# Optimization experiments

Hardware: AMD Instinct MI355X
Metric: run time of the kernel (lower is better)

## Reference

```python
import jax, jax.numpy as jnp
import numpy as np

B, I, J, DIN, DOUT = 256, 1152, 10, 8, 16
ROUTING_ITERS = 3


def squash(v):
    # v: [..., D]; squash(v) = (|v|^2 / (1+|v|^2)) * v/|v| = v * |v| / (1+|v|^2)
    l2 = jnp.linalg.norm(v, axis=-1, keepdims=True)
    return v * (l2 / (1.0 + l2 * l2))


def setup_inputs() -> dict:
    key = jax.random.key(0)
    k1, k2 = jax.random.split(key)
    x = jax.random.normal(k1, (B, I, DIN), dtype=jnp.float32)
    # per-(i,j) Linear(DIN -> DOUT, bias=False) weights, stacked: [I, J, DOUT, DIN]
    W = jax.random.normal(k2, (I, J, DOUT, DIN), dtype=jnp.float32) * 0.1
    return {"x": x, "W": W}


def reference(x, W):
    # prediction vectors u[b,i,j,:] = W[i,j] @ x[b,i,:]  -> [B, I, J, DOUT]
    u = jnp.einsum('bid,ijod->bijo', x, W)
    b = jnp.zeros((I, J), dtype=u.dtype)  # routing logits (shared across batch)
    s = None
    for _ in range(ROUTING_ITERS):
        c = jax.nn.softmax(b, axis=-1)              # [I, J]
        s = jnp.einsum('ij,bijd->bjd', c, u)        # coupling-weighted sum over in-caps
        s = squash(s)                               # [B, J, DOUT]
        # agreement: b[i,j] += sum_b <u[b,i,j], s[b,j]>
        b = b + jnp.einsum('bijd,bjd->ij', u, s)
    return s
```

## Files before the change

### kernel.cpp

```cpp
#include <hip/hip_runtime.h>
#include <math.h>

typedef unsigned short ushort_t;
typedef __attribute__((ext_vector_type(8))) __bf16 bf16x8;
typedef __attribute__((ext_vector_type(4))) float floatx4;

#define B_    256
#define I_    1152
#define J_    10
#define DIN_  8
#define DOUT_ 16
#define K_    (I_*DIN_)
#define N_    (J_*DOUT_)
#define WPS   16
#define KCHUNK (K_/WPS)
#define KSTEPS (KCHUNK/32)

static __device__ __forceinline__ ushort_t f2bf(float f) {
    unsigned int u = __float_as_uint(f);
    u += 0x7fffu + ((u >> 16) & 1u);
    return (ushort_t)(u >> 16);
}
static __device__ __forceinline__ float bf2f(ushort_t h) {
    return __uint_as_float(((unsigned int)h) << 16);
}

__global__ __launch_bounds__(1024)
void gemm_s_fused_kernel(const float* __restrict__ x, const float* __restrict__ W,
                         const float* __restrict__ blog, float* __restrict__ s_out,
                         ushort_t* __restrict__ Sbt_hi, ushort_t* __restrict__ Sbt_lo,
                         const int iter)
{
    const int tid  = threadIdx.x;
    const int tile = blockIdx.x;
    const int lane = tid & 63;
    const int w    = tid >> 6;
    const int mb   = tile / J_;
    const int nt   = tile - mb * J_;

    __shared__ float  c_lds[I_];
    __shared__ floatx4 part[WPS * 64];

    if (iter > 0) {
        for (int r2 = tid; r2 < I_; r2 += 1024) {
            const float* br = blog + (size_t)r2 * J_;
            float bv[J_];
            float mx = -1e30f;
            #pragma unroll
            for (int j = 0; j < J_; ++j) { bv[j] = br[j]; mx = fmaxf(mx, bv[j]); }
            float sum = 0.f;
            #pragma unroll
            for (int j = 0; j < J_; ++j) { bv[j] = __expf(bv[j] - mx); sum += bv[j]; }
            c_lds[r2] = bv[nt] / sum;
        }
        __syncthreads();
    }

    {
        const int r = lane & 15, q = lane >> 4;
        const float* ap = x + (size_t)(mb * 16 + r) * K_ + w * KCHUNK + 8 * q;
        const float* wp = W + (((size_t)(w * 72 + q) * J_ + nt) * DOUT_ + r) * DIN_;
        floatx4 acc = {0.f, 0.f, 0.f, 0.f};
        #pragma unroll
        for (int s = 0; s < KSTEPS; ++s) {
            float4 xa0 = *(const float4*)(ap + s * 32);
            float4 xa1 = *(const float4*)(ap + s * 32 + 4);
            float4 w0  = *(const float4*)(wp + (size_t)s * 4 * J_ * DOUT_ * DIN_);
            float4 w1  = *(const float4*)(wp + (size_t)s * 4 * J_ * DOUT_ * DIN_ + 4);
            float cs   = (iter == 0) ? 0.1f : c_lds[w * 72 + 4 * s + q];
            float xv[8]  = {xa0.x, xa0.y, xa0.z, xa0.w, xa1.x, xa1.y, xa1.z, xa1.w};
            float wvv[8] = {w0.x, w0.y, w0.z, w0.w, w1.x, w1.y, w1.z, w1.w};
            bf16x8 ah, al, bh, bl;
            #pragma unroll
            for (int e = 0; e < 8; ++e) {
                float xe = xv[e];
                __bf16 h = (__bf16)xe;
                ah[e] = h;
                al[e] = (__bf16)(xe - (float)h);
                float pe = wvv[e] * cs;
                __bf16 g = (__bf16)pe;
                bh[e] = g;
                bl[e] = (__bf16)(pe - (float)g);
            }
            acc = __builtin_amdgcn_mfma_f32_16x16x32_bf16(ah, bh, acc, 0, 0, 0);
            acc = __builtin_amdgcn_mfma_f32_16x16x32_bf16(al, bh, acc, 0, 0, 0);
            acc = __builtin_amdgcn_mfma_f32_16x16x32_bf16(ah, bl, acc, 0, 0, 0);
        }
        part[w * 64 + lane] = acc;
    }
    __syncthreads();

    if (tid < 256) {
        const int b_local = tid >> 4;
        const int o       = tid & 15;
        const int lane_c  = ((b_local >> 2) << 4) | o;
        const int reg     = b_local & 3;
        float v = 0.f;
        #pragma unroll
        for (int u = 0; u < WPS; ++u)
            v += part[u * 64 + lane_c][reg];
        float sq = v * v;
        #pragma unroll
        for (int off = 1; off < 16; off <<= 1)
            sq += __shfl_xor(sq, off, 16);
        float l2 = sqrtf(sq);
        float val = v * (l2 / (1.f + sq));
        const int b  = mb * 16 + b_local;
        const int jo = nt * 16 + o;
        if (iter == 2) {
            s_out[(size_t)b * N_ + jo] = val;
        } else {
            ushort_t hi = f2bf(val);
            Sbt_hi[(size_t)jo * B_ + b] = hi;
            Sbt_lo[(size_t)jo * B_ + b] = f2bf(val - bf2f(hi));
        }
    }
}

__global__ __launch_bounds__(256)
void gemm_bupd_kernel(const float* __restrict__ x,
                      const ushort_t* __restrict__ Sbt_hi, const ushort_t* __restrict__ Sbt_lo,
                      const float* __restrict__ W, float* __restrict__ blog,
                      const int first)
{
    int wv   = blockIdx.x * 4 + (threadIdx.x >> 6);
    int lane = threadIdx.x & 63;
    int mt = wv / J_;
    int j  = wv - mt * J_;
    int r = lane & 15, q = lane >> 4;
    const float* xp = x + (size_t)(8 * q) * K_ + (mt * 16 + r);
    size_t boff = (size_t)(j * 16 + r) * B_ + 8 * q;
    floatx4 acc = {0.f, 0.f, 0.f, 0.f};
    #pragma unroll
    for (int s = 0; s < B_ / 32; ++s) {
        bf16x8 ah, al;
        #pragma unroll
        for (int e = 0; e < 8; ++e) {
            float v = xp[(size_t)(s * 32 + e) * K_];
            __bf16 h = (__bf16)v;
            ah[e] = h;
            al[e] = (__bf16)(v - (float)h);
        }
        bf16x8 bh = *(const bf16x8*)(Sbt_hi + boff + s * 32);
        bf16x8 bl = *(const bf16x8*)(Sbt_lo + boff + s * 32);
        acc = __builtin_amdgcn_mfma_f32_16x16x32_bf16(ah, bh, acc, 0, 0, 0);
        acc = __builtin_amdgcn_mfma_f32_16x16x32_bf16(al, bh, acc, 0, 0, 0);
        acc = __builtin_amdgcn_mfma_f32_16x16x32_bf16(ah, bl, acc, 0, 0, 0);
    }
    int i  = mt * 2 + (q >> 1);
    int d0 = (q & 1) * 4;
    int o  = lane & 15;
    const float4 w4 = *(const float4*)(W + ((((size_t)i * J_ + j) * DOUT_ + o) * DIN_ + d0));
    float val = acc[0] * w4.x + acc[1] * w4.y + acc[2] * w4.z + acc[3] * w4.w;
    #pragma unroll
    for (int off = 1; off < 32; off <<= 1)
        val += __shfl_xor(val, off, 32);
    if ((lane & 31) == 0) {
        float* dst = blog + (size_t)(mt * 2 + (lane >> 5)) * J_ + j;
        if (first) *dst = val; else *dst += val;
    }
}

extern "C" void kernel_launch(void* const* d_in, const int* in_sizes, int n_in,
                              void* d_out, int out_size, void* d_ws, size_t ws_size,
                              hipStream_t stream)
{
    const float* x = (const float*)d_in[0];
    const float* W = (const float*)d_in[1];
    float* s_out = (float*)d_out;

    char* ws = (char*)d_ws;
    ushort_t* Sbt_hi = (ushort_t*)(ws);
    ushort_t* Sbt_lo = (ushort_t*)(ws + 81920);
    float*    blog   = (float*)   (ws + 163840);

    for (int it = 0; it < 3; ++it) {
        gemm_s_fused_kernel<<<160, 1024, 0, stream>>>(x, W, blog, s_out,
                                                      Sbt_hi, Sbt_lo, it);
        if (it < 2)
            gemm_bupd_kernel<<<1440, 256, 0, stream>>>(x, Sbt_hi, Sbt_lo,
                                                       W, blog, it == 0 ? 1 : 0);
    }
}
```

Before: 163.3 us.

## Cache bf16-split W across routing iterations and pair j outputs in bupd

```diff
diff --git a/kernel.cpp b/kernel.cpp
--- a/kernel.cpp
+++ b/kernel.cpp
@@ -29,6 +29,7 @@
 void gemm_s_fused_kernel(const float* __restrict__ x, const float* __restrict__ W,
                          const float* __restrict__ blog, float* __restrict__ s_out,
                          ushort_t* __restrict__ Sbt_hi, ushort_t* __restrict__ Sbt_lo,
+                         ushort_t* __restrict__ Wt_hi, ushort_t* __restrict__ Wt_lo,
                          const int iter)
 {
     const int tid  = threadIdx.x;
@@ -60,31 +61,57 @@
         const int r = lane & 15, q = lane >> 4;
         const float* ap = x + (size_t)(mb * 16 + r) * K_ + w * KCHUNK + 8 * q;
         const float* wp = W + (((size_t)(w * 72 + q) * J_ + nt) * DOUT_ + r) * DIN_;
+        const size_t wtoff = (size_t)(nt * 16 + r) * K_ + w * KCHUNK + 8 * q;
         floatx4 acc = {0.f, 0.f, 0.f, 0.f};
-        #pragma unroll
-        for (int s = 0; s < KSTEPS; ++s) {
-            float4 xa0 = *(const float4*)(ap + s * 32);
-            float4 xa1 = *(const float4*)(ap + s * 32 + 4);
-            float4 w0  = *(const float4*)(wp + (size_t)s * 4 * J_ * DOUT_ * DIN_);
-            float4 w1  = *(const float4*)(wp + (size_t)s * 4 * J_ * DOUT_ * DIN_ + 4);
-            float cs   = (iter == 0) ? 0.1f : c_lds[w * 72 + 4 * s + q];
-            float xv[8]  = {xa0.x, xa0.y, xa0.z, xa0.w, xa1.x, xa1.y, xa1.z, xa1.w};
-            float wvv[8] = {w0.x, w0.y, w0.z, w0.w, w1.x, w1.y, w1.z, w1.w};
-            bf16x8 ah, al, bh, bl;
-            #pragma unroll
-            for (int e = 0; e < 8; ++e) {
-                float xe = xv[e];
-                __bf16 h = (__bf16)xe;
-                ah[e] = h;
-                al[e] = (__bf16)(xe - (float)h);
-                float pe = wvv[e] * cs;
-                __bf16 g = (__bf16)pe;
-                bh[e] = g;
-                bl[e] = (__bf16)(pe - (float)g);
+
+        if (iter == 0) {
+            #pragma unroll
+            for (int s = 0; s < KSTEPS; ++s) {
+                float4 xa0 = *(const float4*)(ap + s * 32);
+                float4 xa1 = *(const float4*)(ap + s * 32 + 4);
+                float4 w0  = *(const float4*)(wp + (size_t)s * 4 * J_ * DOUT_ * DIN_);
+                float4 w1  = *(const float4*)(wp + (size_t)s * 4 * J_ * DOUT_ * DIN_ + 4);
+                float xv[8]  = {xa0.x, xa0.y, xa0.z, xa0.w, xa1.x, xa1.y, xa1.z, xa1.w};
+                float wvv[8] = {w0.x, w0.y, w0.z, w0.w, w1.x, w1.y, w1.z, w1.w};
+                bf16x8 ah, al, bh, bl;
+                #pragma unroll
+                for (int e = 0; e < 8; ++e) {
+                    float xe = xv[e] * 0.1f;
+                    __bf16 h = (__bf16)xe;
+                    ah[e] = h;
+                    al[e] = (__bf16)(xe - (float)h);
+                    float pe = wvv[e];
+                    __bf16 g = (__bf16)pe;
+                    bh[e] = g;
+                    bl[e] = (__bf16)(pe - (float)g);
+                }
+                *(bf16x8*)(Wt_hi + wtoff + s * 32) = bh;
+                *(bf16x8*)(Wt_lo + wtoff + s * 32) = bl;
+                acc = __builtin_amdgcn_mfma_f32_16x16x32_bf16(ah, bh, acc, 0, 0, 0);
+                acc = __builtin_amdgcn_mfma_f32_16x16x32_bf16(al, bh, acc, 0, 0, 0);
+                acc = __builtin_amdgcn_mfma_f32_16x16x32_bf16(ah, bl, acc, 0, 0, 0);
             }
-            acc = __builtin_amdgcn_mfma_f32_16x16x32_bf16(ah, bh, acc, 0, 0, 0);
-            acc = __builtin_amdgcn_mfma_f32_16x16x32_bf16(al, bh, acc, 0, 0, 0);
-            acc = __builtin_amdgcn_mfma_f32_16x16x32_bf16(ah, bl, acc, 0, 0, 0);
+        } else {
+            #pragma unroll
+            for (int s = 0; s < KSTEPS; ++s) {
+                float4 xa0 = *(const float4*)(ap + s * 32);
+                float4 xa1 = *(const float4*)(ap + s * 32 + 4);
+                bf16x8 bh = *(const bf16x8*)(Wt_hi + wtoff + s * 32);
+                bf16x8 bl = *(const bf16x8*)(Wt_lo + wtoff + s * 32);
+                float cs  = c_lds[w * 72 + 4 * s + q];
+                float xv[8] = {xa0.x, xa0.y, xa0.z, xa0.w, xa1.x, xa1.y, xa1.z, xa1.w};
+                bf16x8 ah, al;
+                #pragma unroll
+                for (int e = 0; e < 8; ++e) {
+                    float xe = xv[e] * cs;
+                    __bf16 h = (__bf16)xe;
+                    ah[e] = h;
+                    al[e] = (__bf16)(xe - (float)h);
+                }
+                acc = __builtin_amdgcn_mfma_f32_16x16x32_bf16(ah, bh, acc, 0, 0, 0);
+                acc = __builtin_amdgcn_mfma_f32_16x16x32_bf16(al, bh, acc, 0, 0, 0);
+                acc = __builtin_amdgcn_mfma_f32_16x16x32_bf16(ah, bl, acc, 0, 0, 0);
+            }
         }
         part[w * 64 + lane] = acc;
     }
@@ -125,12 +152,15 @@
 {
     int wv   = blockIdx.x * 4 + (threadIdx.x >> 6);
     int lane = threadIdx.x & 63;
-    int mt = wv / J_;
-    int j  = wv - mt * J_;
+    int mt = wv / 5;
+    int jp = wv - mt * 5;
+    int j0 = jp * 2, j1 = jp * 2 + 1;
     int r = lane & 15, q = lane >> 4;
     const float* xp = x + (size_t)(8 * q) * K_ + (mt * 16 + r);
-    size_t boff = (size_t)(j * 16 + r) * B_ + 8 * q;
-    floatx4 acc = {0.f, 0.f, 0.f, 0.f};
+    size_t b0off = (size_t)(j0 * 16 + r) * B_ + 8 * q;
+    size_t b1off = (size_t)(j1 * 16 + r) * B_ + 8 * q;
+    floatx4 acc0 = {0.f, 0.f, 0.f, 0.f};
+    floatx4 acc1 = {0.f, 0.f, 0.f, 0.f};
     #pragma unroll
     for (int s = 0; s < B_ / 32; ++s) {
         bf16x8 ah, al;
@@ -141,23 +171,42 @@
             ah[e] = h;
             al[e] = (__bf16)(v - (float)h);
         }
-        bf16x8 bh = *(const bf16x8*)(Sbt_hi + boff + s * 32);
-        bf16x8 bl = *(const bf16x8*)(Sbt_lo + boff + s * 32);
-        acc = __builtin_amdgcn_mfma_f32_16x16x32_bf16(ah, bh, acc, 0, 0, 0);
-        acc = __builtin_amdgcn_mfma_f32_16x16x32_bf16(al, bh, acc, 0, 0, 0);
-        acc = __builtin_amdgcn_mfma_f32_16x16x32_bf16(ah, bl, acc, 0, 0, 0);
+        bf16x8 bh0 = *(const bf16x8*)(Sbt_hi + b0off + s * 32);
+        bf16x8 bl0 = *(const bf16x8*)(Sbt_lo + b0off + s * 32);
+        bf16x8 bh1 = *(const bf16x8*)(Sbt_hi + b1off + s * 32);
+        bf16x8 bl1 = *(const bf16x8*)(Sbt_lo + b1off + s * 32);
+        acc0 = __builtin_amdgcn_mfma_f32_16x16x32_bf16(ah, bh0, acc0, 0, 0, 0);
+        acc0 = __builtin_amdgcn_mfma_f32_16x16x32_bf16(al, bh0, acc0, 0, 0, 0);
+        acc0 = __builtin_amdgcn_mfma_f32_16x16x32_bf16(ah, bl0, acc0, 0, 0, 0);
+        acc1 = __builtin_amdgcn_mfma_f32_16x16x32_bf16(ah, bh1, acc1, 0, 0, 0);
+        acc1 = __builtin_amdgcn_mfma_f32_16x16x32_bf16(al, bh1, acc1, 0, 0, 0);
+        acc1 = __builtin_amdgcn_mfma_f32_16x16x32_bf16(ah, bl1, acc1, 0, 0, 0);
     }
     int i  = mt * 2 + (q >> 1);
     int d0 = (q & 1) * 4;
     int o  = lane & 15;
-    const float4 w4 = *(const float4*)(W + ((((size_t)i * J_ + j) * DOUT_ + o) * DIN_ + d0));
-    float val = acc[0] * w4.x + acc[1] * w4.y + acc[2] * w4.z + acc[3] * w4.w;
-    #pragma unroll
-    for (int off = 1; off < 32; off <<= 1)
-        val += __shfl_xor(val, off, 32);
-    if ((lane & 31) == 0) {
-        float* dst = blog + (size_t)(mt * 2 + (lane >> 5)) * J_ + j;
-        if (first) *dst = val; else *dst += val;
+    int iw = mt * 2 + (lane >> 5);
+    {
+        const float4 w4 = *(const float4*)(W + ((((size_t)i * J_ + j0) * DOUT_ + o) * DIN_ + d0));
+        float val = acc0[0] * w4.x + acc0[1] * w4.y + acc0[2] * w4.z + acc0[3] * w4.w;
+        #pragma unroll
+        for (int off = 1; off < 32; off <<= 1)
+            val += __shfl_xor(val, off, 32);
+        if ((lane & 31) == 0) {
+            float* dst = blog + (size_t)iw * J_ + j0;
+            if (first) *dst = val; else *dst += val;
+        }
+    }
+    {
+        const float4 w4 = *(const float4*)(W + ((((size_t)i * J_ + j1) * DOUT_ + o) * DIN_ + d0));
+        float val = acc1[0] * w4.x + acc1[1] * w4.y + acc1[2] * w4.z + acc1[3] * w4.w;
+        #pragma unroll
+        for (int off = 1; off < 32; off <<= 1)
+            val += __shfl_xor(val, off, 32);
+        if ((lane & 31) == 0) {
+            float* dst = blog + (size_t)iw * J_ + j1;
+            if (first) *dst = val; else *dst += val;
+        }
     }
 }
 
@@ -173,12 +222,15 @@
     ushort_t* Sbt_hi = (ushort_t*)(ws);
     ushort_t* Sbt_lo = (ushort_t*)(ws + 81920);
     float*    blog   = (float*)   (ws + 163840);
+    ushort_t* Wt_hi  = (ushort_t*)(ws + 209920);
+    ushort_t* Wt_lo  = (ushort_t*)(ws + 3159040);
 
     for (int it = 0; it < 3; ++it) {
         gemm_s_fused_kernel<<<160, 1024, 0, stream>>>(x, W, blog, s_out,
-                                                      Sbt_hi, Sbt_lo, it);
+                                                      Sbt_hi, Sbt_lo,
+                                                      Wt_hi, Wt_lo, it);
         if (it < 2)
-            gemm_bupd_kernel<<<1440, 256, 0, stream>>>(x, Sbt_hi, Sbt_lo,
-                                                       W, blog, it == 0 ? 1 : 0);
-    }
-}
+            gemm_bupd_kernel<<<720, 256, 0, stream>>>(x, Sbt_hi, Sbt_lo,
+                                                      W, blog, it == 0 ? 1 : 0);
+    }
+}
```

Result: slower. 199.6 us (+22.2%).

## Fuse routing-logit update into s-computation kernel with atomic accumulation

Applied to the files above, without the earlier changes.

```diff
diff --git a/kernel.cpp b/kernel.cpp
--- a/kernel.cpp
+++ b/kernel.cpp
@@ -26,9 +26,8 @@
 }
 
 __global__ __launch_bounds__(1024)
-void gemm_s_fused_kernel(const float* __restrict__ x, const float* __restrict__ W,
-                         const float* __restrict__ blog, float* __restrict__ s_out,
-                         ushort_t* __restrict__ Sbt_hi, ushort_t* __restrict__ Sbt_lo,
+void capsule_iter_kernel(const float* __restrict__ x, const float* __restrict__ W,
+                         float* __restrict__ blog, float* __restrict__ s_out,
                          const int iter)
 {
     const int tid  = threadIdx.x;
@@ -37,9 +36,12 @@
     const int w    = tid >> 6;
     const int mb   = tile / J_;
     const int nt   = tile - mb * J_;
+    const int b0   = mb * 16;
+    const int r    = lane & 15, q = lane >> 4;
 
-    __shared__ float  c_lds[I_];
+    __shared__ float   c_lds[I_];
     __shared__ floatx4 part[WPS * 64];
+    __shared__ float   s_lds[16 * 16];
 
     if (iter > 0) {
         for (int r2 = tid; r2 < I_; r2 += 1024) {
@@ -57,7 +59,6 @@
     }
 
     {
-        const int r = lane & 15, q = lane >> 4;
         const float* ap = x + (size_t)(mb * 16 + r) * K_ + w * KCHUNK + 8 * q;
         const float* wp = W + (((size_t)(w * 72 + q) * J_ + nt) * DOUT_ + r) * DIN_;
         floatx4 acc = {0.f, 0.f, 0.f, 0.f};
@@ -105,59 +106,60 @@
             sq += __shfl_xor(sq, off, 16);
         float l2 = sqrtf(sq);
         float val = v * (l2 / (1.f + sq));
-        const int b  = mb * 16 + b_local;
-        const int jo = nt * 16 + o;
-        if (iter == 2) {
-            s_out[(size_t)b * N_ + jo] = val;
-        } else {
-            ushort_t hi = f2bf(val);
-            Sbt_hi[(size_t)jo * B_ + b] = hi;
-            Sbt_lo[(size_t)jo * B_ + b] = f2bf(val - bf2f(hi));
+        if (iter == 2)
+            s_out[(size_t)(b0 + b_local) * N_ + nt * 16 + o] = val;
+        else
+            s_lds[b_local * 16 + o] = val;
+    }
+
+    if (iter == 2) return;
+    __syncthreads();
+
+    {
+        bf16x8 bh, bl;
+        #pragma unroll
+        for (int e = 0; e < 8; ++e) { bh[e] = (__bf16)0.f; bl[e] = (__bf16)0.f; }
+        if (q < 2) {
+            #pragma unroll
+            for (int e = 0; e < 8; ++e) {
+                float sv = s_lds[(8 * q + e) * 16 + r];
+                __bf16 h = (__bf16)sv;
+                bh[e] = h;
+                bl[e] = (__bf16)(sv - (float)h);
+            }
         }
-    }
-}
-
-__global__ __launch_bounds__(256)
-void gemm_bupd_kernel(const float* __restrict__ x,
-                      const ushort_t* __restrict__ Sbt_hi, const ushort_t* __restrict__ Sbt_lo,
-                      const float* __restrict__ W, float* __restrict__ blog,
-                      const int first)
-{
-    int wv   = blockIdx.x * 4 + (threadIdx.x >> 6);
-    int lane = threadIdx.x & 63;
-    int mt = wv / J_;
-    int j  = wv - mt * J_;
-    int r = lane & 15, q = lane >> 4;
-    const float* xp = x + (size_t)(8 * q) * K_ + (mt * 16 + r);
-    size_t boff = (size_t)(j * 16 + r) * B_ + 8 * q;
-    floatx4 acc = {0.f, 0.f, 0.f, 0.f};
-    #pragma unroll
-    for (int s = 0; s < B_ / 32; ++s) {
-        bf16x8 ah, al;
-        #pragma unroll
-        for (int e = 0; e < 8; ++e) {
-            float v = xp[(size_t)(s * 32 + e) * K_];
-            __bf16 h = (__bf16)v;
-            ah[e] = h;
-            al[e] = (__bf16)(v - (float)h);
+        for (int mtl = 0; mtl < 36; ++mtl) {
+            const int mt = w * 36 + mtl;
+            bf16x8 ah, al;
+            #pragma unroll
+            for (int e = 0; e < 8; ++e) { ah[e] = (__bf16)0.f; al[e] = (__bf16)0.f; }
+            if (q < 2) {
+                const float* xp = x + (size_t)(b0 + 8 * q) * K_ + mt * 16 + r;
+                #pragma unroll
+                for (int e = 0; e < 8; ++e) {
+                    float v = xp[(size_t)e * K_];
+                    __bf16 h = (__bf16)v;
+                    ah[e] = h;
+                    al[e] = (__bf16)(v - (float)h);
+                }
+            }
+            floatx4 accd = {0.f, 0.f, 0.f, 0.f};
+            accd = __builtin_amdgcn_mfma_f32_16x16x32_bf16(ah, bh, accd, 0, 0, 0);
+            accd = __builtin_amdgcn_mfma_f32_16x16x32_bf16(al, bh, accd, 0, 0, 0);
+            accd = __builtin_amdgcn_mfma_f32_16x16x32_bf16(ah, bl, accd, 0, 0, 0);
+            const int i  = mt * 2 + (q >> 1);
+            const int d0 = (q & 1) * 4;
+            const int o  = lane & 15;
+            const float4 w4 = *(const float4*)(W +
+                ((((size_t)i * J_ + nt) * DOUT_ + o) * DIN_ + d0));
+            float val = accd[0] * w4.x + accd[1] * w4.y
+                      + accd[2] * w4.z + accd[3] * w4.w;
+            #pragma unroll
+            for (int off = 1; off < 32; off <<= 1)
+                val += __shfl_xor(val, off, 32);
+            if ((lane & 31) == 0)
+                atomicAdd(blog + (size_t)(mt * 2 + (lane >> 5)) * J_ + nt, val);
         }
-        bf16x8 bh = *(const bf16x8*)(Sbt_hi + boff + s * 32);
-        bf16x8 bl = *(const bf16x8*)(Sbt_lo + boff + s * 32);
-        acc = __builtin_amdgcn_mfma_f32_16x16x32_bf16(ah, bh, acc, 0, 0, 0);
-        acc = __builtin_amdgcn_mfma_f32_16x16x32_bf16(al, bh, acc, 0, 0, 0);
-        acc = __builtin_amdgcn_mfma_f32_16x16x32_bf16(ah, bl, acc, 0, 0, 0);
-    }
-    int i  = mt * 2 + (q >> 1);
-    int d0 = (q & 1) * 4;
-    int o  = lane & 15;
-    const float4 w4 = *(const float4*)(W + ((((size_t)i * J_ + j) * DOUT_ + o) * DIN_ + d0));
-    float val = acc[0] * w4.x + acc[1] * w4.y + acc[2] * w4.z + acc[3] * w4.w;
-    #pragma unroll
-    for (int off = 1; off < 32; off <<= 1)
-        val += __shfl_xor(val, off, 32);
-    if ((lane & 31) == 0) {
-        float* dst = blog + (size_t)(mt * 2 + (lane >> 5)) * J_ + j;
-        if (first) *dst = val; else *dst += val;
     }
 }
 
@@ -168,17 +170,9 @@
     const float* x = (const float*)d_in[0];
     const float* W = (const float*)d_in[1];
     float* s_out = (float*)d_out;
+    float* blog  = (float*)d_ws;
 
-    char* ws = (char*)d_ws;
-    ushort_t* Sbt_hi = (ushort_t*)(ws);
-    ushort_t* Sbt_lo = (ushort_t*)(ws + 81920);
-    float*    blog   = (float*)   (ws + 163840);
-
-    for (int it = 0; it < 3; ++it) {
-        gemm_s_fused_kernel<<<160, 1024, 0, stream>>>(x, W, blog, s_out,
-                                                      Sbt_hi, Sbt_lo, it);
-        if (it < 2)
-            gemm_bupd_kernel<<<1440, 256, 0, stream>>>(x, Sbt_hi, Sbt_lo,
-                                                       W, blog, it == 0 ? 1 : 0);
-    }
+    hipMemsetAsync(blog, 0, (size_t)I_ * J_ * sizeof(float), stream);
+    for (int it = 0; it < 3; ++it)
+        capsule_iter_kernel<<<160, 1024, 0, stream>>>(x, W, blog, s_out, it);
 }
```

After: 212.0 us. 1.3x slower.
